# Performance work log

Hardware: AMD Instinct MI355X
Metric: run time of the kernel (lower is better)

The kernel has to match this reference:

```python
import jax, jax.numpy as jnp
from jax import lax
import numpy as np

P = 32      # num_series
H = 128     # hidden units
B = 32      # batch
T = 256     # sequence length

def setup_inputs() -> dict:
    key = jax.random.key(0)
    ks = jax.random.split(key, 8)
    s = 1.0 / np.sqrt(H)
    X     = jax.random.normal(ks[0], (B, T, P), dtype=jnp.float32)
    # per-network LSTM weights, PyTorch gate order (i, f, g, o) stacked in 4H
    W_ih  = jax.random.uniform(ks[1], (P, 4 * H, P), dtype=jnp.float32, minval=-s, maxval=s)
    W_hh  = jax.random.uniform(ks[2], (P, 4 * H, H), dtype=jnp.float32, minval=-s, maxval=s)
    b_ih  = jax.random.uniform(ks[3], (P, 4 * H), dtype=jnp.float32, minval=-s, maxval=s)
    b_hh  = jax.random.uniform(ks[4], (P, 4 * H), dtype=jnp.float32, minval=-s, maxval=s)
    # Conv1d(hidden, 1, kernel_size=1) == per-timestep linear H -> 1, per network
    W_out = jax.random.uniform(ks[5], (P, H), dtype=jnp.float32, minval=-s, maxval=s)
    b_out = jax.random.uniform(ks[6], (P,), dtype=jnp.float32, minval=-s, maxval=s)
    return {"X": X, "W_ih": W_ih, "W_hh": W_hh, "b_ih": b_ih,
            "b_hh": b_hh, "W_out": W_out, "b_out": b_out}

def reference(X, W_ih, W_hh, b_ih, b_hh, W_out, b_out):
    # X: (B, T, P); p independent 1-layer LSTMs run on the same input,
    # batched along a network axis n (size P) with distinct weights.
    # Precompute input projections for all steps/networks: (T, B, P, 4H)
    xproj = jnp.einsum('btd,nkd->tbnk', X, W_ih) + b_ih + b_hh

    def step(carry, xp_t):
        h, c = carry                                   # (B, P, H) each
        gates = xp_t + jnp.einsum('bnh,nkh->bnk', h, W_hh)
        i, f, g, o = jnp.split(gates, 4, axis=-1)
        i = jax.nn.sigmoid(i)
        f = jax.nn.sigmoid(f)
        g = jnp.tanh(g)
        o = jax.nn.sigmoid(o)
        c = f * c + i * g
        h = o * jnp.tanh(c)
        return (h, c), h

    h0 = jnp.zeros((X.shape[0], W_ih.shape[0], W_hh.shape[2]), X.dtype)
    (_, _), hs = lax.scan(step, (h0, h0), xproj)        # hs: (T, B, P, H)
    # 1x1 conv head per network, then concat over networks -> (B, T, P)
    pred = jnp.einsum('tbnh,nh->btn', hs, W_out) + b_out
    return pred
```

## Files before the change

kernel.cpp:

```cpp
#include <hip/hip_runtime.h>
#include <stdint.h>

#define NP 32
#define NH 128
#define NB 32
#define NT 256
#define FH 512

typedef __attribute__((ext_vector_type(4))) float float4_t;
typedef __attribute__((ext_vector_type(8))) __bf16 bf16x8;

static __device__ __forceinline__ float4_t mfma_bf16(bf16x8 a, bf16x8 b, float4_t c) {
  return __builtin_amdgcn_mfma_f32_16x16x32_bf16(a, b, c, 0, 0, 0);
}

#define LOG2E 1.4426950408889634f

#define BAR() __asm__ volatile("s_waitcnt lgkmcnt(0)\n\ts_barrier" ::: "memory")

__global__ __launch_bounds__(512, 1) void clstm_fused(
    const float* __restrict__ X, const float* __restrict__ Wih,
    const float* __restrict__ Whh, const float* __restrict__ bih,
    const float* __restrict__ bhh, const float* __restrict__ Wout,
    const float* __restrict__ bout, float* __restrict__ out)
{
  const int net = blockIdx.x >> 3, bq = blockIdx.x & 7;
  const int tid = threadIdx.x;
  const int w = tid >> 6, lane = tid & 63;
  const int quad = lane >> 4, l16 = lane & 15;

  __shared__ __bf16 hfrag[2][4][4][4][8];

  {
    ((int*)hfrag)[tid] = 0;
  }
  __syncthreads();

  bf16x8 bfrag[4][5];
  float4_t bias4[4];
#pragma unroll
  for (int g = 0; g < 4; ++g) {
    const float scale = (g == 2) ? (-2.0f*LOG2E) : (-LOG2E);
    const int col = g*NH + w*16 + l16;
#pragma unroll
    for (int kc = 0; kc < 5; ++kc) {
      const float* src = (kc == 0) ? (Wih + ((size_t)net*FH + col)*NP + quad*8)
                                   : (Whh + ((size_t)net*FH + col)*NH + (kc-1)*32 + quad*8);
      bf16x8 bf;
#pragma unroll
      for (int j = 0; j < 8; ++j) bf[j] = (__bf16)(src[j] * scale);
      bfrag[g][kc] = bf;
    }
    const float b = (bih[net*FH + col] + bhh[net*FH + col]) * scale;
    bias4[g] = (float4_t){b, b, b, b};
  }

  bf16x8 wof[4];
#pragma unroll
  for (int kc = 0; kc < 4; ++kc) {
    const float* wp = Wout + net*NH + kc*32 + quad*8;
#pragma unroll
    for (int j = 0; j < 8; ++j) wof[kc][j] = (__bf16)wp[j];
  }
  const float bo = bout[net];

  float cs = 0.f;
  const float S2 = -2.0f*LOG2E;

  const float* xrow = X + (size_t)(bq*4 + (l16 & 3))*(NT*NP) + quad*8;

  const int kcp = w >> 1, q2 = ((w & 1) << 1) | (l16 >> 3), jj = l16 & 7;

  float* outp = out + ((size_t)bq*4)*(NT*NP) + net;

  bf16x8 ax;
  {
    float xv0[8];
    *(float4_t*)&xv0[0] = *(const float4_t*)xrow;
    *(float4_t*)&xv0[4] = *(const float4_t*)(xrow + 4);
#pragma unroll
    for (int j = 0; j < 8; ++j) ax[j] = (__bf16)xv0[j];
  }
  const float* xp = xrow + NP;
  float xv[8] = {0.f,0.f,0.f,0.f,0.f,0.f,0.f,0.f};

  for (int t = 0; t < NT; ++t) {
    const int rd = t & 1, wr = rd ^ 1;

    bf16x8 ah[4];
#pragma unroll
    for (int kc = 0; kc < 4; ++kc)
      ah[kc] = *(const bf16x8*)&hfrag[rd][kc][quad][l16 & 3][0];

    float4_t accx[4];
#pragma unroll
    for (int g = 0; g < 4; ++g)
      accx[g] = mfma_bf16(ax, bfrag[g][0], bias4[g]);

    if (t + 1 < NT) {
      *(float4_t*)&xv[0] = *(const float4_t*)xp;
      *(float4_t*)&xv[4] = *(const float4_t*)(xp + 4);
    }

    float4_t acc[4];
#pragma unroll
    for (int g = 0; g < 4; ++g) {
      float4_t a0 = mfma_bf16(ah[0], bfrag[g][1], accx[g]);
      float4_t a1 = mfma_bf16(ah[2], bfrag[g][3], (float4_t){0.f,0.f,0.f,0.f});
      a0 = mfma_bf16(ah[1], bfrag[g][2], a0);
      a1 = mfma_bf16(ah[3], bfrag[g][4], a1);
      acc[g] = a0 + a1;
    }

    float gv[4];
#pragma unroll
    for (int g = 0; g < 4; ++g) {
      float a01 = (quad & 1) ? acc[g][1] : acc[g][0];
      float a23 = (quad & 1) ? acc[g][3] : acc[g][2];
      gv[g] = (quad & 2) ? a23 : a01;
    }

    float h;
    {
      float ei = __builtin_amdgcn_exp2f(gv[0]);
      float ig = __builtin_amdgcn_rcpf(1.0f + ei);
      float ef = __builtin_amdgcn_exp2f(gv[1]);
      float fg = __builtin_amdgcn_rcpf(1.0f + ef);
      float eg = __builtin_amdgcn_exp2f(fminf(gv[2], 126.0f));
      float rg = __builtin_amdgcn_rcpf(1.0f + eg);
      float t0 = S2 * rg;
      float gg2 = t0 - t0 * eg;
      float eo = __builtin_amdgcn_exp2f(gv[3]);
      float og = __builtin_amdgcn_rcpf(1.0f + eo);
      cs = fg * cs + ig * gg2;
      float ec = __builtin_amdgcn_exp2f(fminf(cs, 126.0f));
      float rc = __builtin_amdgcn_rcpf(1.0f + ec);
      float th = rc - ec * rc;
      h = og * th;
    }

    hfrag[wr][kcp][q2][quad][jj] = (__bf16)h;

    if (w == 0 && t > 0) {
      float4_t p0 = {bo, bo, bo, bo};
      float4_t p1 = {0.f, 0.f, 0.f, 0.f};
      p0 = mfma_bf16(ah[0], wof[0], p0);
      p1 = mfma_bf16(ah[2], wof[2], p1);
      p0 = mfma_bf16(ah[1], wof[1], p0);
      p1 = mfma_bf16(ah[3], wof[3], p1);
      float4_t po = p0 + p1;
      if (lane == 0) {
#pragma unroll
        for (int r = 0; r < 4; ++r)
          outp[(size_t)r*(NT*NP) + (t - 1)*NP] = po[r];
      }
    }

#pragma unroll
    for (int j = 0; j < 8; ++j) ax[j] = (__bf16)xv[j];
    xp += NP;

    BAR();
  }

  if (w == 0) {
    bf16x8 ahf[4];
#pragma unroll
    for (int kc = 0; kc < 4; ++kc)
      ahf[kc] = *(const bf16x8*)&hfrag[NT & 1][kc][quad][l16 & 3][0];
    float4_t p0 = {bo, bo, bo, bo};
    float4_t p1 = {0.f, 0.f, 0.f, 0.f};
    p0 = mfma_bf16(ahf[0], wof[0], p0);
    p1 = mfma_bf16(ahf[2], wof[2], p1);
    p0 = mfma_bf16(ahf[1], wof[1], p0);
    p1 = mfma_bf16(ahf[3], wof[3], p1);
    float4_t po = p0 + p1;
    if (lane == 0) {
#pragma unroll
      for (int r = 0; r < 4; ++r)
        outp[(size_t)r*(NT*NP) + (NT - 1)*NP] = po[r];
    }
  }
}

extern "C" void kernel_launch(void* const* d_in, const int* in_sizes, int n_in,
                              void* d_out, int out_size, void* d_ws, size_t ws_size,
                              hipStream_t stream) {
  const float* X    = (const float*)d_in[0];
  const float* Wih  = (const float*)d_in[1];
  const float* Whh  = (const float*)d_in[2];
  const float* bih  = (const float*)d_in[3];
  const float* bhh  = (const float*)d_in[4];
  const float* Wout = (const float*)d_in[5];
  const float* bout = (const float*)d_in[6];
  float* out = (float*)d_out;
  (void)in_sizes; (void)n_in; (void)out_size; (void)d_ws; (void)ws_size;

  clstm_fused<<<256, 512, 0, stream>>>(X, Wih, Whh, bih, bhh, Wout, bout, out);
}
```

Before: 257.5 us.

## Halve block size to 4 waves, each computing two 16-unit hidden tiles

```diff
diff --git a/kernel.cpp b/kernel.cpp
--- a/kernel.cpp
+++ b/kernel.cpp
@@ -18,7 +18,7 @@
 
 #define BAR() __asm__ volatile("s_waitcnt lgkmcnt(0)\n\ts_barrier" ::: "memory")
 
-__global__ __launch_bounds__(512, 1) void clstm_fused(
+__global__ __launch_bounds__(256, 1) void clstm_fused(
     const float* __restrict__ X, const float* __restrict__ Wih,
     const float* __restrict__ Whh, const float* __restrict__ bih,
     const float* __restrict__ bhh, const float* __restrict__ Wout,
@@ -32,27 +32,30 @@
   __shared__ __bf16 hfrag[2][4][4][4][8];
 
   {
-    ((int*)hfrag)[tid] = 0;
+    ((int*)hfrag)[2*tid] = 0; ((int*)hfrag)[2*tid+1] = 0;
   }
   __syncthreads();
 
-  bf16x8 bfrag[4][5];
-  float4_t bias4[4];
-#pragma unroll
-  for (int g = 0; g < 4; ++g) {
-    const float scale = (g == 2) ? (-2.0f*LOG2E) : (-LOG2E);
-    const int col = g*NH + w*16 + l16;
-#pragma unroll
-    for (int kc = 0; kc < 5; ++kc) {
-      const float* src = (kc == 0) ? (Wih + ((size_t)net*FH + col)*NP + quad*8)
-                                   : (Whh + ((size_t)net*FH + col)*NH + (kc-1)*32 + quad*8);
-      bf16x8 bf;
-#pragma unroll
-      for (int j = 0; j < 8; ++j) bf[j] = (__bf16)(src[j] * scale);
-      bfrag[g][kc] = bf;
-    }
-    const float b = (bih[net*FH + col] + bhh[net*FH + col]) * scale;
-    bias4[g] = (float4_t){b, b, b, b};
+  bf16x8 bfrag[2][4][5];
+  float4_t bias4[2][4];
+#pragma unroll
+  for (int ut = 0; ut < 2; ++ut) {
+#pragma unroll
+    for (int g = 0; g < 4; ++g) {
+      const float scale = (g == 2) ? (-2.0f*LOG2E) : (-LOG2E);
+      const int col = g*NH + 32*w + 16*ut + l16;
+#pragma unroll
+      for (int kc = 0; kc < 5; ++kc) {
+        const float* src = (kc == 0) ? (Wih + ((size_t)net*FH + col)*NP + quad*8)
+                                     : (Whh + ((size_t)net*FH + col)*NH + (kc-1)*32 + quad*8);
+        bf16x8 bf;
+#pragma unroll
+        for (int j = 0; j < 8; ++j) bf[j] = (__bf16)(src[j] * scale);
+        bfrag[ut][g][kc] = bf;
+      }
+      const float b = (bih[net*FH + col] + bhh[net*FH + col]) * scale;
+      bias4[ut][g] = (float4_t){b, b, b, b};
+    }
   }
 
   bf16x8 wof[4];
@@ -63,13 +66,15 @@
     for (int j = 0; j < 8; ++j) wof[kc][j] = (__bf16)wp[j];
   }
   const float bo = bout[net];
-
-  float cs = 0.f;
+  const float4_t bo4 = {bo, bo, bo, bo};
+  const float4_t z4  = {0.f, 0.f, 0.f, 0.f};
+
+  float cs0 = 0.f, cs1 = 0.f;
   const float S2 = -2.0f*LOG2E;
 
   const float* xrow = X + (size_t)(bq*4 + (l16 & 3))*(NT*NP) + quad*8;
 
-  const int kcp = w >> 1, q2 = ((w & 1) << 1) | (l16 >> 3), jj = l16 & 7;
+  const int q2lo = l16 >> 3, jj = l16 & 7;
 
   float* outp = out + ((size_t)bq*4)*(NT*NP) + net;
 
@@ -92,60 +97,82 @@
     for (int kc = 0; kc < 4; ++kc)
       ah[kc] = *(const bf16x8*)&hfrag[rd][kc][quad][l16 & 3][0];
 
-    float4_t accx[4];
-#pragma unroll
-    for (int g = 0; g < 4; ++g)
-      accx[g] = mfma_bf16(ax, bfrag[g][0], bias4[g]);
+    float4_t accx[2][4];
+#pragma unroll
+    for (int ut = 0; ut < 2; ++ut)
+#pragma unroll
+      for (int g = 0; g < 4; ++g)
+        accx[ut][g] = mfma_bf16(ax, bfrag[ut][g][0], bias4[ut][g]);
 
     if (t + 1 < NT) {
       *(float4_t*)&xv[0] = *(const float4_t*)xp;
       *(float4_t*)&xv[4] = *(const float4_t*)(xp + 4);
     }
 
-    float4_t acc[4];
+    float4_t acc[2][4];
+#pragma unroll
+    for (int ut = 0; ut < 2; ++ut) {
+#pragma unroll
+      for (int g = 0; g < 4; ++g) {
+        float4_t a0 = mfma_bf16(ah[0], bfrag[ut][g][1], accx[ut][g]);
+        float4_t a1 = mfma_bf16(ah[2], bfrag[ut][g][3], z4);
+        a0 = mfma_bf16(ah[1], bfrag[ut][g][2], a0);
+        a1 = mfma_bf16(ah[3], bfrag[ut][g][4], a1);
+        acc[ut][g] = a0 + a1;
+      }
+    }
+
+    float gv0[4], gv1[4];
 #pragma unroll
     for (int g = 0; g < 4; ++g) {
-      float4_t a0 = mfma_bf16(ah[0], bfrag[g][1], accx[g]);
-      float4_t a1 = mfma_bf16(ah[2], bfrag[g][3], (float4_t){0.f,0.f,0.f,0.f});
-      a0 = mfma_bf16(ah[1], bfrag[g][2], a0);
-      a1 = mfma_bf16(ah[3], bfrag[g][4], a1);
-      acc[g] = a0 + a1;
-    }
-
-    float gv[4];
-#pragma unroll
-    for (int g = 0; g < 4; ++g) {
-      float a01 = (quad & 1) ? acc[g][1] : acc[g][0];
-      float a23 = (quad & 1) ? acc[g][3] : acc[g][2];
-      gv[g] = (quad & 2) ? a23 : a01;
-    }
-
-    float h;
+      float a01 = (quad & 1) ? acc[0][g][1] : acc[0][g][0];
+      float a23 = (quad & 1) ? acc[0][g][3] : acc[0][g][2];
+      gv0[g] = (quad & 2) ? a23 : a01;
+      float b01 = (quad & 1) ? acc[1][g][1] : acc[1][g][0];
+      float b23 = (quad & 1) ? acc[1][g][3] : acc[1][g][2];
+      gv1[g] = (quad & 2) ? b23 : b01;
+    }
+
+    float h0, h1;
     {
-      float ei = __builtin_amdgcn_exp2f(gv[0]);
+      float ei = __builtin_amdgcn_exp2f(gv0[0]);
       float ig = __builtin_amdgcn_rcpf(1.0f + ei);
-      float ef = __builtin_amdgcn_exp2f(gv[1]);
+      float ef = __builtin_amdgcn_exp2f(gv0[1]);
       float fg = __builtin_amdgcn_rcpf(1.0f + ef);
-      float eg = __builtin_amdgcn_exp2f(fminf(gv[2], 126.0f));
+      float eg = __builtin_amdgcn_exp2f(fminf(gv0[2], 126.0f));
       float rg = __builtin_amdgcn_rcpf(1.0f + eg);
       float t0 = S2 * rg;
       float gg2 = t0 - t0 * eg;
-      float eo = __builtin_amdgcn_exp2f(gv[3]);
+      float eo = __builtin_amdgcn_exp2f(gv0[3]);
       float og = __builtin_amdgcn_rcpf(1.0f + eo);
-      cs = fg * cs + ig * gg2;
-      float ec = __builtin_amdgcn_exp2f(fminf(cs, 126.0f));
+      cs0 = fg * cs0 + ig * gg2;
+      float ec = __builtin_amdgcn_exp2f(fminf(cs0, 126.0f));
       float rc = __builtin_amdgcn_rcpf(1.0f + ec);
-      float th = rc - ec * rc;
-      h = og * th;
-    }
-
-    hfrag[wr][kcp][q2][quad][jj] = (__bf16)h;
+      h0 = og * (rc - ec * rc);
+    }
+    {
+      float ei = __builtin_amdgcn_exp2f(gv1[0]);
+      float ig = __builtin_amdgcn_rcpf(1.0f + ei);
+      float ef = __builtin_amdgcn_exp2f(gv1[1]);
+      float fg = __builtin_amdgcn_rcpf(1.0f + ef);
+      float eg = __builtin_amdgcn_exp2f(fminf(gv1[2], 126.0f));
+      float rg = __builtin_amdgcn_rcpf(1.0f + eg);
+      float t0 = S2 * rg;
+      float gg2 = t0 - t0 * eg;
+      float eo = __builtin_amdgcn_exp2f(gv1[3]);
+      float og = __builtin_amdgcn_rcpf(1.0f + eo);
+      cs1 = fg * cs1 + ig * gg2;
+      float ec = __builtin_amdgcn_exp2f(fminf(cs1, 126.0f));
+      float rc = __builtin_amdgcn_rcpf(1.0f + ec);
+      h1 = og * (rc - ec * rc);
+    }
+
+    hfrag[wr][w][q2lo    ][quad][jj] = (__bf16)h0;
+    hfrag[wr][w][q2lo + 2][quad][jj] = (__bf16)h1;
 
     if (w == 0 && t > 0) {
-      float4_t p0 = {bo, bo, bo, bo};
-      float4_t p1 = {0.f, 0.f, 0.f, 0.f};
-      p0 = mfma_bf16(ah[0], wof[0], p0);
-      p1 = mfma_bf16(ah[2], wof[2], p1);
+      float4_t p0 = mfma_bf16(ah[0], wof[0], bo4);
+      float4_t p1 = mfma_bf16(ah[2], wof[2], z4);
       p0 = mfma_bf16(ah[1], wof[1], p0);
       p1 = mfma_bf16(ah[3], wof[3], p1);
       float4_t po = p0 + p1;
@@ -168,10 +195,8 @@
 #pragma unroll
     for (int kc = 0; kc < 4; ++kc)
       ahf[kc] = *(const bf16x8*)&hfrag[NT & 1][kc][quad][l16 & 3][0];
-    float4_t p0 = {bo, bo, bo, bo};
-    float4_t p1 = {0.f, 0.f, 0.f, 0.f};
-    p0 = mfma_bf16(ahf[0], wof[0], p0);
-    p1 = mfma_bf16(ahf[2], wof[2], p1);
+    float4_t p0 = mfma_bf16(ahf[0], wof[0], bo4);
+    float4_t p1 = mfma_bf16(ahf[2], wof[2], z4);
     p0 = mfma_bf16(ahf[1], wof[1], p0);
     p1 = mfma_bf16(ahf[3], wof[3], p1);
     float4_t po = p0 + p1;
@@ -196,5 +221,5 @@
   float* out = (float*)d_out;
   (void)in_sizes; (void)n_in; (void)out_size; (void)d_ws; (void)ws_size;
 
-  clstm_fused<<<256, 512, 0, stream>>>(X, Wih, Whh, bih, bhh, Wout, bout, out);
+  clstm_fused<<<256, 256, 0, stream>>>(X, Wih, Whh, bih, bhh, Wout, bout, out);
 }
```

After: 303.9 us. 18.0% more time.
